# Performance work log

Measured on AMD Instinct MI355X. Metric: run time of the kernel, lower is better.

The kernel has to match this reference:

```python
import jax, jax.numpy as jnp
import numpy as np

B, N, C, H, R, E = 64, 512, 64, 8, 17, 21
HD = C // H
BETA = 0.01


def setup_inputs() -> dict:
    key = jax.random.key(0)
    ks = jax.random.split(key, 13)
    s = 0.02
    x = jax.random.normal(ks[0], (B, N, C), jnp.float32)
    ext = jax.random.normal(ks[1], (B, N, E), jnp.float32)
    # soft sector-assignment tensor (dense float, as used by the einsum)
    assignment = jax.random.uniform(ks[2], (N, N, R), jnp.float32)
    mask = jax.random.randint(ks[3], (N, R), 0, 2) == 1
    mask = mask.at[:, 0].set(False)  # guarantee >=1 unmasked sector per node
    Wq = jax.random.normal(ks[4], (C, C), jnp.float32) * s
    Wkv = jax.random.normal(ks[5], (2 * C, C), jnp.float32) * s
    relative_bias = jax.random.normal(ks[6], (H, 1, R), jnp.float32)
    W1 = jax.random.normal(ks[7], (64, E), jnp.float32) * s
    b1 = jnp.zeros((64,), jnp.float32)
    W2 = jax.random.normal(ks[8], (H * R, 64), jnp.float32) * s
    b2 = jnp.zeros((H * R,), jnp.float32)
    Wp = jax.random.normal(ks[9], (C, C), jnp.float32) * s
    bp = jnp.zeros((C,), jnp.float32)
    return dict(x=x, ext=ext, assignment=assignment, Wq=Wq, Wkv=Wkv,
                relative_bias=relative_bias, W1=W1, b1=b1, W2=W2, b2=b2,
                Wp=Wp, bp=bp, mask=mask)


def reference(x, ext, assignment, Wq, Wkv, relative_bias, W1, b1, W2, b2, Wp, bp, mask):
    scale = HD ** (-0.5)
    # sector gather: [B,N,C] x [N,N,R] -> [B,N,R,C]
    pre_kv = jnp.einsum('bnc,mnr->bmrc', x, assignment)
    # projections (torch Linear: y = x @ W^T)
    q = (x @ Wq.T).reshape(B, N, H, HD)                 # per-token single query
    kv = pre_kv @ Wkv.T                                  # [B,N,R,2C]
    k, v = jnp.split(kv, 2, axis=-1)
    k = k.reshape(B, N, R, H, HD)
    v = v.reshape(B, N, R, H, HD)
    # tiny 1xR attention per (b,n,h)
    attn = jnp.einsum('bnhd,bnrhd->bnhr', q, k) * scale
    attn = attn + relative_bias[:, 0, :][None, None]     # [H,R] broadcast
    # ext modulation
    ext_imp = jax.nn.relu(ext @ W1.T + b1) @ W2.T + b2   # [B,N,H*R] (dropout=eval)
    attn = attn + BETA * ext_imp.reshape(B, N, H, R)
    attn = jnp.where(mask[None, :, None, :], -jnp.inf, attn)
    p = jax.nn.softmax(attn, axis=-1)
    out = jnp.einsum('bnhr,bnrhd->bnhd', p, v).reshape(B, N, C)
    return out @ Wp.T + bp
```

## Files before the change

kernel.cpp:

```cpp
#include <hip/hip_runtime.h>
#include <hip/hip_bf16.h>

typedef __bf16 bf16x8 __attribute__((ext_vector_type(8)));
typedef float f32x4 __attribute__((ext_vector_type(4)));

#define NN 512
#define NR 17

#define SWZ(row, b) (((((b) >> 4) ^ ((row) & 7)) << 4) | ((b) & 15))

__device__ __forceinline__ __bf16 f2b(float f) {
  __hip_bfloat16 h = __float2bfloat16(f);
  return __builtin_bit_cast(__bf16, h);
}

__device__ __forceinline__ void gload_lds16(const void* g, void* l) {
  __builtin_amdgcn_global_load_lds(
      (const __attribute__((address_space(1))) void*)g,
      (__attribute__((address_space(3))) void*)l, 16, 0, 0);
}

__global__ __launch_bounds__(256) void pack_A(const float* __restrict__ a,
                                              __hip_bfloat16* __restrict__ A2) {
  __shared__ __hip_bfloat16 T[NR * 136];
  const int m = blockIdx.y;
  const int n0 = blockIdx.x * 128;
  const float* src = a + (size_t)m * (NN * NR) + (size_t)n0 * NR;
  for (int t = threadIdx.x; t < 128 * NR; t += 256) {
    int i = t / NR;
    int r = t - i * NR;
    T[r * 136 + i] = __float2bfloat16(src[t]);
  }
  __syncthreads();
  for (int t = threadIdx.x; t < NR * 128; t += 256) {
    int r = t >> 7;
    int i = t & 127;
    A2[((size_t)m * NR + r) * NN + n0 + i] = T[r * 136 + i];
  }
}

__global__ __launch_bounds__(256) void pack_X(const float* __restrict__ x,
                                              __hip_bfloat16* __restrict__ XT,
                                              __hip_bfloat16* __restrict__ XR) {
  __shared__ __hip_bfloat16 T[64 * 136];
  const int by = blockIdx.y;
  const int n0 = blockIdx.x * 128;
  const float* src = x + ((size_t)by * NN + n0) * 64;
  for (int t = threadIdx.x; t < 128 * 64; t += 256) {
    int i = t >> 6;
    int c = t & 63;
    __hip_bfloat16 v = __float2bfloat16(src[t]);
    T[c * 136 + i] = v;
    XR[((size_t)by * NN + n0 + i) * 64 + c] = v;
  }
  __syncthreads();
  for (int t = threadIdx.x; t < 64 * 128; t += 256) {
    int c = t >> 7;
    int i = t & 127;
    XT[((size_t)by * 64 + c) * NN + n0 + i] = T[c * 136 + i];
  }
}

__global__ __launch_bounds__(256) void prep_w(const float* __restrict__ Wq,
                                              const float* __restrict__ Wkv,
                                              const float* __restrict__ Wp,
                                              __hip_bfloat16* __restrict__ WQK,
                                              __hip_bfloat16* __restrict__ WVP) {
  const int base = blockIdx.x * 512 + threadIdx.x;
#pragma unroll
  for (int k = 0; k < 2; ++k) {
    const int idx = base + k * 256;
    {
      const int i = idx & 63, row = idx >> 6, h = row >> 6, c = row & 63;
      float a = 0.f;
#pragma unroll
      for (int d = 0; d < 8; ++d) a += Wq[(h * 8 + d) * 64 + i] * Wkv[(h * 8 + d) * 64 + c];
      WQK[idx] = __float2bfloat16(a * 0.35355339059327373f);
    }
    {
      const int hc = idx & 511, j = idx >> 9, h = hc >> 6, c = hc & 63;
      float a = 0.f;
#pragma unroll
      for (int d = 0; d < 8; ++d)
        a += Wkv[4096 + (h * 8 + d) * 64 + c] * Wp[j * 64 + (h * 8 + d)];
      WVP[idx] = __float2bfloat16(a);
    }
  }
}

#define PREKV_NWG 2176
__global__ __launch_bounds__(256) void gemm_prekv(const __hip_bfloat16* __restrict__ A2,
                                                  const __hip_bfloat16* __restrict__ XT,
                                                  __hip_bfloat16* __restrict__ pkv) {
  __shared__ char As[16384];
  __shared__ char Bs[16384];
  const int tid = threadIdx.x;
  const int wave = tid >> 6;
  const int lane = tid & 63;
  const int flat = blockIdx.y * gridDim.x + blockIdx.x;
  const int s = (flat & 7) * (PREKV_NWG / 8) + (flat >> 3);
  const int rowBase = (s >> 5) * 128;
  const int colBase = (s & 31) * 128;
  const int wrow0 = (wave >> 1) * 64;
  const int wcol0 = (wave & 1) * 64;
  const int lrow8 = lane >> 3;
  const int gslot = lane & 7;
  const int gsrc = gslot ^ lrow8;

  f32x4 acc[4][4];
#pragma unroll
  for (int i = 0; i < 4; ++i)
#pragma unroll
    for (int j = 0; j < 4; ++j) acc[i][j] = (f32x4)0.0f;

  const int fr = lane & 15;
  const int kg = lane >> 4;

  for (int kt = 0; kt < NN; kt += 64) {
#pragma unroll
    for (int cc = 0; cc < 4; ++cc) {
      const int r0 = wave * 32 + cc * 8;
      gload_lds16(A2 + ((size_t)(rowBase + r0 + lrow8) * NN + kt + gsrc * 8), As + r0 * 128);
      gload_lds16(XT + ((size_t)(colBase + r0 + lrow8) * NN + kt + gsrc * 8), Bs + r0 * 128);
    }
    __syncthreads();
#pragma unroll
    for (int kk = 0; kk < 2; ++kk) {
      bf16x8 av[4], bv[4];
#pragma unroll
      for (int mi = 0; mi < 4; ++mi) {
        const int row = wrow0 + mi * 16 + fr;
        const int slot = (kk * 4 + kg) ^ (row & 7);
        av[mi] = *(const bf16x8*)(As + row * 128 + slot * 16);
      }
#pragma unroll
      for (int ni = 0; ni < 4; ++ni) {
        const int row = wcol0 + ni * 16 + fr;
        const int slot = (kk * 4 + kg) ^ (row & 7);
        bv[ni] = *(const bf16x8*)(Bs + row * 128 + slot * 16);
      }
#pragma unroll
      for (int mi = 0; mi < 4; ++mi)
#pragma unroll
        for (int ni = 0; ni < 4; ++ni)
          acc[mi][ni] =
              __builtin_amdgcn_mfma_f32_16x16x32_bf16(av[mi], bv[ni], acc[mi][ni], 0, 0, 0);
    }
    __syncthreads();
  }

  const int rq = lane >> 4;
#pragma unroll
  for (int mi = 0; mi < 4; ++mi) {
#pragma unroll
    for (int ni = 0; ni < 4; ++ni) {
#pragma unroll
      for (int reg = 0; reg < 4; ++reg) {
        const int gi = rowBase + wrow0 + mi * 16 + rq * 4 + reg;
        const int gj = colBase + wcol0 + ni * 16 + fr;
        const unsigned m = (unsigned)gi / 17u;
        const unsigned r = (unsigned)gi - m * 17u;
        const int bb = gj >> 6;
        const int c = gj & 63;
        pkv[(((size_t)bb * NN + m) * NR + r) * 64 + c] = __float2bfloat16(acc[mi][ni][reg]);
      }
    }
  }
}

__global__ __launch_bounds__(256) void ei_kernel(const float* __restrict__ ext,
                                                 const float* __restrict__ W1p,
                                                 const float* __restrict__ b1p,
                                                 const float* __restrict__ W2p,
                                                 const float* __restrict__ b2p,
                                                 const float* __restrict__ rbp,
                                                 const int* __restrict__ maskp,
                                                 float* __restrict__ EIF) {
  __shared__ float exts[64 * 21];
  __shared__ float W1s[64 * 21];
  __shared__ __hip_bfloat16 Hl[64 * 72];
  const int tid = threadIdx.x;
  const int tblk = blockIdx.x * 64;
  for (int i = tid; i < 64 * 21; i += 256) {
    exts[i] = ext[(size_t)tblk * 21 + i];
    W1s[i] = W1p[i];
  }
  __syncthreads();
  const int wave = tid >> 6, lane = tid & 63;
#pragma unroll
  for (int k = 0; k < 16; ++k) {
    const int tl = k * 4 + wave;
    float a = b1p[lane];
#pragma unroll
    for (int e = 0; e < 21; ++e) a += exts[tl * 21 + e] * W1s[lane * 21 + e];
    Hl[tl * 72 + lane] = __float2bfloat16(fmaxf(a, 0.f));
  }
  __syncthreads();
  const int fr = lane & 15, kg = lane >> 4;
  const __bf16* Hb = (const __bf16*)Hl;
  bf16x8 a0 = *(const bf16x8*)(Hb + (wave * 16 + fr) * 72 + kg * 8);
  bf16x8 a1 = *(const bf16x8*)(Hb + (wave * 16 + fr) * 72 + 32 + kg * 8);
#pragma unroll
  for (int tile = 0; tile < 9; ++tile) {
    const int o = tile * 16 + fr;
    bf16x8 bv0 = (bf16x8)f2b(0.0f), bv1 = (bf16x8)f2b(0.0f);
    if (o < 136) {
#pragma unroll
      for (int jj = 0; jj < 8; ++jj) {
        bv0[jj] = f2b(W2p[o * 64 + kg * 8 + jj]);
        bv1[jj] = f2b(W2p[o * 64 + 32 + kg * 8 + jj]);
      }
    }
    f32x4 acc = (f32x4)0.0f;
    acc = __builtin_amdgcn_mfma_f32_16x16x32_bf16(a0, bv0, acc, 0, 0, 0);
    acc = __builtin_amdgcn_mfma_f32_16x16x32_bf16(a1, bv1, acc, 0, 0, 0);
    if (o < 136) {
      const int h = (o * 241) >> 12;
      const int r = o - h * 17;
      const float rbo = rbp[o], b2o = b2p[o];
#pragma unroll
      for (int reg = 0; reg < 4; ++reg) {
        const int tl = tblk + wave * 16 + kg * 4 + reg;
        const int m = tl & (NN - 1);
        float v = maskp[m * NR + r] ? -1e30f : (rbo + 0.01f * (acc[reg] + b2o));
        EIF[(size_t)tl * 136 + o] = v;
      }
    }
  }
}

__global__ __launch_bounds__(256, 2) void attn_mega(
    const __hip_bfloat16* __restrict__ XRp, const __hip_bfloat16* __restrict__ WQKp,
    const __hip_bfloat16* __restrict__ WVPp, const __hip_bfloat16* __restrict__ pkvB,
    const float* __restrict__ eifB, const float* __restrict__ bpp,
    float* __restrict__ outp) {
  extern __shared__ char smem[];
  char* qws = smem;
  char* Ts = smem + 32768;
  const int tid = threadIdx.x;
  const int wave = tid >> 6;
  const int lane = tid & 63;
  const int fr = lane & 15;
  const int kg = lane >> 4;
  const int t0 = blockIdx.x * 32;
  char* pT = smem + 65536 + wave * 4096;

  {
    const int rt = wave >> 1;
    const int ct0 = (wave & 1) * 16;
    bf16x8 a0 = *(const bf16x8*)((const __bf16*)XRp + (size_t)(t0 + rt * 16 + fr) * 64 + kg * 8);
    bf16x8 a1 =
        *(const bf16x8*)((const __bf16*)XRp + (size_t)(t0 + rt * 16 + fr) * 64 + 32 + kg * 8);
#pragma unroll
    for (int ci = 0; ci < 16; ++ci) {
      const int ct = ct0 + ci;
      f32x4 acc = (f32x4)0.0f;
      bf16x8 b0 = *(const bf16x8*)((const __bf16*)WQKp + (size_t)(ct * 16 + fr) * 64 + kg * 8);
      bf16x8 b1 =
          *(const bf16x8*)((const __bf16*)WQKp + (size_t)(ct * 16 + fr) * 64 + 32 + kg * 8);
      acc = __builtin_amdgcn_mfma_f32_16x16x32_bf16(a0, b0, acc, 0, 0, 0);
      acc = __builtin_amdgcn_mfma_f32_16x16x32_bf16(a1, b1, acc, 0, 0, 0);
#pragma unroll
      for (int reg = 0; reg < 4; ++reg) {
        const int row = rt * 16 + kg * 4 + reg;
        const int col = ct * 16 + fr;
        *(__hip_bfloat16*)(qws + row * 1024 + SWZ(row, col * 2)) = __float2bfloat16(acc[reg]);
      }
    }
  }

  {
    bf16x8 z = (bf16x8)f2b(0.0f);
#pragma unroll
    for (int j = 0; j < 4; ++j) *(bf16x8*)(pT + lane * 64 + j * 16) = z;
  }
  __syncthreads();

  for (int i = 0; i < 8; ++i) {
    const int tl = wave * 8 + i;
    const size_t tg = (size_t)t0 + tl;
    const __bf16* pk = (const __bf16*)pkvB + tg * 1088;

    bf16x8 v0 = *(const bf16x8*)(pk + lane * 8);
    bf16x8 v1 = *(const bf16x8*)(pk + 512 + lane * 8);
    __bf16 vt = pk[1024 + lane];
    {
      const int r0 = lane >> 3;
      const int cb = (lane & 7) * 8;
#pragma unroll
      for (int j = 0; j < 8; ++j) {
        const int c = cb + j;
        const int sl0 = (0 ^ ((c >> 2) & 3)) << 4;
        const int sl1 = (1 ^ ((c >> 2) & 3)) << 4;
        *(__bf16*)(pT + c * 64 + sl0 + r0 * 2) = v0[j];
        *(__bf16*)(pT + c * 64 + sl1 + r0 * 2) = v1[j];
      }
      const int c = lane;
      *(__bf16*)(pT + c * 64 + ((2 ^ ((c >> 2) & 3)) << 4)) = vt;
    }

    f32x4 slo = (f32x4)0.0f, shi = (f32x4)0.0f;
#pragma unroll
    for (int kk = 0; kk < 2; ++kk) {
      const int g = fr * 8 + kk * 4 + kg;
      bf16x8 av = *(const bf16x8*)(qws + tl * 1024 + ((g ^ (tl & 7)) << 4));
      bf16x8 blo = *(const bf16x8*)(pk + fr * 64 + kk * 32 + kg * 8);
      bf16x8 bhi = (bf16x8)f2b(0.0f);
      if (fr == 0) bhi = *(const bf16x8*)(pk + 1024 + kk * 32 + kg * 8);
      slo = __builtin_amdgcn_mfma_f32_16x16x32_bf16(av, blo, slo, 0, 0, 0);
      shi = __builtin_amdgcn_mfma_f32_16x16x32_bf16(av, bhi, shi, 0, 0, 0);
    }

    const float* eif = eifB + tg * 136;
    float plo[4], phi[4];
#pragma unroll
    for (int reg = 0; reg < 4; ++reg) {
      const int h = kg * 4 + reg;
      float llo = slo[reg] + eif[h * 17 + fr];
      float lhi = (fr == 0) ? (shi[reg] + eif[h * 17 + 16]) : -1e30f;
      float mx = fmaxf(llo, lhi);
      mx = fmaxf(mx, __shfl_xor(mx, 1));
      mx = fmaxf(mx, __shfl_xor(mx, 2));
      mx = fmaxf(mx, __shfl_xor(mx, 4));
      mx = fmaxf(mx, __shfl_xor(mx, 8));
      float el = __expf(llo - mx);
      float eh = __expf(lhi - mx);
      float sm = el + eh;
      sm += __shfl_xor(sm, 1);
      sm += __shfl_xor(sm, 2);
      sm += __shfl_xor(sm, 4);
      sm += __shfl_xor(sm, 8);
      const float iv = 1.0f / sm;
      plo[reg] = el * iv;
      phi[reg] = eh * iv;
    }

#pragma unroll
    for (int reg = 0; reg < 4; ++reg) {
      const int h = kg * 4 + reg;
      *(__hip_bfloat16*)(Ts + tl * 1024 + SWZ(tl, (h * 32 + fr) * 2)) =
          __float2bfloat16(plo[reg]);
      *(__hip_bfloat16*)(Ts + tl * 1024 + SWZ(tl, (h * 32 + 16 + fr) * 2)) =
          __float2bfloat16(phi[reg]);
    }
    bf16x8 ap = *(const bf16x8*)(Ts + tl * 1024 + (((fr * 4 + kg) ^ (tl & 7)) << 4));

#pragma unroll
    for (int ni = 0; ni < 4; ++ni) {
      const int c = ni * 16 + fr;
      bf16x8 bv = *(const bf16x8*)(pT + c * 64 + ((kg ^ ((c >> 2) & 3)) << 4));
      f32x4 o = __builtin_amdgcn_mfma_f32_16x16x32_bf16(ap, bv, (f32x4)0.0f, 0, 0, 0);
      if (kg < 2) {
#pragma unroll
        for (int reg = 0; reg < 4; ++reg) {
          const int h = kg * 4 + reg;
          *(__hip_bfloat16*)(Ts + tl * 1024 + SWZ(tl, (h * 64 + c) * 2)) =
              __float2bfloat16(o[reg]);
        }
      }
    }
  }
  __syncthreads();

  {
    const int rt = wave >> 1;
    const int ct_base = (wave & 1) * 2;
#pragma unroll
    for (int cj = 0; cj < 2; ++cj) {
      const int ct = ct_base + cj;
      f32x4 acc = (f32x4)0.0f;
#pragma unroll
      for (int kk = 0; kk < 16; ++kk) {
        const int row = rt * 16 + fr;
        bf16x8 a = *(const bf16x8*)(Ts + row * 1024 + (((kk * 4 + kg) ^ (row & 7)) << 4));
        bf16x8 b = *(const bf16x8*)((const __bf16*)WVPp + (size_t)(ct * 16 + fr) * 512 +
                                    kk * 32 + kg * 8);
        acc = __builtin_amdgcn_mfma_f32_16x16x32_bf16(a, b, acc, 0, 0, 0);
      }
      const float bpv = bpp[ct * 16 + fr];
#pragma unroll
      for (int reg = 0; reg < 4; ++reg)
        outp[(size_t)(t0 + rt * 16 + kg * 4 + reg) * 64 + ct * 16 + fr] = acc[reg] + bpv;
    }
  }
}

extern "C" void kernel_launch(void* const* d_in, const int* in_sizes, int n_in, void* d_out,
                              int out_size, void* d_ws, size_t ws_size, hipStream_t stream) {
  const float* x = (const float*)d_in[0];
  const float* ext = (const float*)d_in[1];
  const float* assign = (const float*)d_in[2];
  const float* Wq = (const float*)d_in[3];
  const float* Wkv = (const float*)d_in[4];
  const float* rb = (const float*)d_in[5];
  const float* W1 = (const float*)d_in[6];
  const float* b1 = (const float*)d_in[7];
  const float* W2 = (const float*)d_in[8];
  const float* b2 = (const float*)d_in[9];
  const float* Wp = (const float*)d_in[10];
  const float* bp = (const float*)d_in[11];
  const int* mask = (const int*)d_in[12];
  float* out = (float*)d_out;

  char* ws = (char*)d_ws;
  __hip_bfloat16* A2 = (__hip_bfloat16*)(ws + 0);
  __hip_bfloat16* WQK = (__hip_bfloat16*)(ws + 8912896);
  __hip_bfloat16* WVP = (__hip_bfloat16*)(ws + 8978432);
  __hip_bfloat16* XT = (__hip_bfloat16*)(ws + 9043968);
  __hip_bfloat16* XR = (__hip_bfloat16*)(ws + 13238272);
  __hip_bfloat16* PKV = (__hip_bfloat16*)(ws + 17432576);
  float* EIF = (float*)(ws + 88735744);
  if (ws_size < (size_t)106565632) return;

  hipLaunchKernelGGL(pack_A, dim3(4, 512), dim3(256), 0, stream, assign, A2);
  hipLaunchKernelGGL(prep_w, dim3(64), dim3(256), 0, stream, Wq, Wkv, Wp, WQK, WVP);
  hipLaunchKernelGGL(pack_X, dim3(4, 64), dim3(256), 0, stream, x, XT, XR);
  hipLaunchKernelGGL(gemm_prekv, dim3(32, 68), dim3(256), 0, stream, A2, XT, PKV);
  hipLaunchKernelGGL(ei_kernel, dim3(512), dim3(256), 0, stream, ext, W1, b1, W2, b2, rb, mask,
                     EIF);
  hipFuncSetAttribute((const void*)attn_mega, hipFuncAttributeMaxDynamicSharedMemorySize, 81920);
  hipLaunchKernelGGL(attn_mega, dim3(1024), dim3(256), 81920, stream, XR, WQK, WVP, PKV, EIF, bp,
                     out);
}
```

Before: 266.5 us.

## Skip masked sector rows in pre-KV GEMM and restructure attention kernel

Adds a mask-scan kernel that compacts the unmasked (node, sector) rows into an index list, and the pre-KV GEMM now computes only those rows, roughly halving its work. The attention kernel is rewritten to handle 16 tokens per block with static shared memory and 4 blocks per CU. It uses register-resident score and PV MFMAs with shuffles instead of an LDS transpose, and prefetches the next token's K/V rows. The ext-bias buffer becomes bf16 with a relayout to cut traffic. Masked rows of PKV are no longer written, so correctness relies on the -1e30 bias zeroing their probabilities and on those stale rows holding no NaN or Inf from previous workspace contents.

```diff
diff --git a/kernel.cpp b/kernel.cpp
--- a/kernel.cpp
+++ b/kernel.cpp
@@ -9,9 +9,15 @@
 
 #define SWZ(row, b) (((((b) >> 4) ^ ((row) & 7)) << 4) | ((b) & 15))
 
+__device__ __forceinline__ float bf2f(__hip_bfloat16 v) { return __bfloat162float(v); }
 __device__ __forceinline__ __bf16 f2b(float f) {
   __hip_bfloat16 h = __float2bfloat16(f);
   return __builtin_bit_cast(__bf16, h);
+}
+__device__ __forceinline__ unsigned pkbf(float a, float b) {
+  unsigned ua = (unsigned)__builtin_bit_cast(unsigned short, __float2bfloat16(a));
+  unsigned ub = (unsigned)__builtin_bit_cast(unsigned short, __float2bfloat16(b));
+  return ua | (ub << 16);
 }
 
 __device__ __forceinline__ void gload_lds16(const void* g, void* l) {
@@ -88,25 +94,63 @@
   }
 }
 
-#define PREKV_NWG 2176
+__global__ __launch_bounds__(512) void mask_scan(const int* __restrict__ maskp,
+                                                 int* __restrict__ rowsp,
+                                                 int* __restrict__ metap) {
+  __shared__ int sc[512];
+  const int tid = threadIdx.x;
+  int c = 0;
+#pragma unroll
+  for (int r = 0; r < NR; ++r) c += (maskp[tid * NR + r] == 0) ? 1 : 0;
+  sc[tid] = c;
+  __syncthreads();
+  for (int s = 1; s < 512; s <<= 1) {
+    int v = (tid >= s) ? sc[tid - s] : 0;
+    __syncthreads();
+    sc[tid] += v;
+    __syncthreads();
+  }
+  int idx = sc[tid] - c;
+#pragma unroll
+  for (int r = 0; r < NR; ++r)
+    if (maskp[tid * NR + r] == 0) rowsp[idx++] = tid * NR + r;
+  if (tid == 511) {
+    const int total = sc[511];
+    const int padded = (total + 127) & ~127;
+    for (int i = total; i < padded; ++i) rowsp[i] = 0;
+    metap[0] = padded;
+  }
+}
+
 __global__ __launch_bounds__(256) void gemm_prekv(const __hip_bfloat16* __restrict__ A2,
                                                   const __hip_bfloat16* __restrict__ XT,
+                                                  const int* __restrict__ rowsp,
+                                                  const int* __restrict__ metap,
                                                   __hip_bfloat16* __restrict__ pkv) {
   __shared__ char As[16384];
   __shared__ char Bs[16384];
+  const int padded = metap[0];
+  const int nwg = (padded >> 7) * 32;
+  const int flat = blockIdx.y * gridDim.x + blockIdx.x;
+  if (flat >= nwg) return;
+  const int s = (flat & 7) * (nwg >> 3) + (flat >> 3);
+  const int rowBase = (s >> 5) * 128;
+  const int colBase = (s & 31) * 128;
+
   const int tid = threadIdx.x;
   const int wave = tid >> 6;
   const int lane = tid & 63;
-  const int flat = blockIdx.y * gridDim.x + blockIdx.x;
-  const int s = (flat & 7) * (PREKV_NWG / 8) + (flat >> 3);
-  const int rowBase = (s >> 5) * 128;
-  const int colBase = (s & 31) * 128;
   const int wrow0 = (wave >> 1) * 64;
   const int wcol0 = (wave & 1) * 64;
   const int lrow8 = lane >> 3;
   const int gslot = lane & 7;
   const int gsrc = gslot ^ lrow8;
 
+  int arow[4];
+#pragma unroll
+  for (int cc = 0; cc < 4; ++cc)
+    arow[cc] = rowsp[rowBase + wave * 32 + cc * 8 + lrow8];
+
   f32x4 acc[4][4];
 #pragma unroll
   for (int i = 0; i < 4; ++i)
@@ -120,7 +164,7 @@
 #pragma unroll
     for (int cc = 0; cc < 4; ++cc) {
       const int r0 = wave * 32 + cc * 8;
-      gload_lds16(A2 + ((size_t)(rowBase + r0 + lrow8) * NN + kt + gsrc * 8), As + r0 * 128);
+      gload_lds16(A2 + ((size_t)arow[cc] * NN + kt + gsrc * 8), As + r0 * 128);
       gload_lds16(XT + ((size_t)(colBase + r0 + lrow8) * NN + kt + gsrc * 8), Bs + r0 * 128);
     }
     __syncthreads();
@@ -157,9 +201,10 @@
 #pragma unroll
       for (int reg = 0; reg < 4; ++reg) {
         const int gi = rowBase + wrow0 + mi * 16 + rq * 4 + reg;
+        const int grow = rowsp[gi];
+        const unsigned m = (unsigned)grow / 17u;
+        const unsigned r = (unsigned)grow - m * 17u;
         const int gj = colBase + wcol0 + ni * 16 + fr;
-        const unsigned m = (unsigned)gi / 17u;
-        const unsigned r = (unsigned)gi - m * 17u;
         const int bb = gj >> 6;
         const int c = gj & 63;
         pkv[(((size_t)bb * NN + m) * NR + r) * 64 + c] = __float2bfloat16(acc[mi][ni][reg]);
@@ -175,7 +220,7 @@
                                                  const float* __restrict__ b2p,
                                                  const float* __restrict__ rbp,
                                                  const int* __restrict__ maskp,
-                                                 float* __restrict__ EIF) {
+                                                 __hip_bfloat16* __restrict__ EIF) {
   __shared__ float exts[64 * 21];
   __shared__ float W1s[64 * 21];
   __shared__ __hip_bfloat16 Hl[64 * 72];
@@ -217,43 +262,40 @@
     if (o < 136) {
       const int h = (o * 241) >> 12;
       const int r = o - h * 17;
+      const int noff = (r < 16) ? ((r >> 2) * 64 + h * 4 + (r & 3)) : (256 + h);
       const float rbo = rbp[o], b2o = b2p[o];
 #pragma unroll
       for (int reg = 0; reg < 4; ++reg) {
         const int tl = tblk + wave * 16 + kg * 4 + reg;
         const int m = tl & (NN - 1);
         float v = maskp[m * NR + r] ? -1e30f : (rbo + 0.01f * (acc[reg] + b2o));
-        EIF[(size_t)tl * 136 + o] = v;
-      }
-    }
-  }
-}
-
-__global__ __launch_bounds__(256, 2) void attn_mega(
+        EIF[(size_t)tl * 272 + noff] = __float2bfloat16(v);
+      }
+    }
+  }
+}
+
+__global__ __launch_bounds__(256, 4) void attn_mega(
     const __hip_bfloat16* __restrict__ XRp, const __hip_bfloat16* __restrict__ WQKp,
     const __hip_bfloat16* __restrict__ WVPp, const __hip_bfloat16* __restrict__ pkvB,
-    const float* __restrict__ eifB, const float* __restrict__ bpp,
+    const __hip_bfloat16* __restrict__ eifB, const float* __restrict__ bpp,
     float* __restrict__ outp) {
-  extern __shared__ char smem[];
-  char* qws = smem;
-  char* Ts = smem + 32768;
+  __shared__ char qws[16 * 1024];
+  __shared__ char Ts[16 * 1024];
   const int tid = threadIdx.x;
   const int wave = tid >> 6;
   const int lane = tid & 63;
   const int fr = lane & 15;
   const int kg = lane >> 4;
-  const int t0 = blockIdx.x * 32;
-  char* pT = smem + 65536 + wave * 4096;
+  const int h8 = fr & 7;
+  const int t0 = blockIdx.x * 16;
 
   {
-    const int rt = wave >> 1;
-    const int ct0 = (wave & 1) * 16;
-    bf16x8 a0 = *(const bf16x8*)((const __bf16*)XRp + (size_t)(t0 + rt * 16 + fr) * 64 + kg * 8);
-    bf16x8 a1 =
-        *(const bf16x8*)((const __bf16*)XRp + (size_t)(t0 + rt * 16 + fr) * 64 + 32 + kg * 8);
-#pragma unroll
-    for (int ci = 0; ci < 16; ++ci) {
-      const int ct = ct0 + ci;
+    bf16x8 a0 = *(const bf16x8*)((const __bf16*)XRp + (size_t)(t0 + fr) * 64 + kg * 8);
+    bf16x8 a1 = *(const bf16x8*)((const __bf16*)XRp + (size_t)(t0 + fr) * 64 + 32 + kg * 8);
+#pragma unroll
+    for (int ci = 0; ci < 8; ++ci) {
+      const int ct = wave * 8 + ci;
       f32x4 acc = (f32x4)0.0f;
       bf16x8 b0 = *(const bf16x8*)((const __bf16*)WQKp + (size_t)(ct * 16 + fr) * 64 + kg * 8);
       bf16x8 b1 =
@@ -262,100 +304,101 @@
       acc = __builtin_amdgcn_mfma_f32_16x16x32_bf16(a1, b1, acc, 0, 0, 0);
 #pragma unroll
       for (int reg = 0; reg < 4; ++reg) {
-        const int row = rt * 16 + kg * 4 + reg;
+        const int row = kg * 4 + reg;
         const int col = ct * 16 + fr;
         *(__hip_bfloat16*)(qws + row * 1024 + SWZ(row, col * 2)) = __float2bfloat16(acc[reg]);
       }
     }
   }
+  __syncthreads();
 
   {
-    bf16x8 z = (bf16x8)f2b(0.0f);
-#pragma unroll
-    for (int j = 0; j < 4; ++j) *(bf16x8*)(pT + lane * 64 + j * 16) = z;
-  }
-  __syncthreads();
-
-  for (int i = 0; i < 8; ++i) {
-    const int tl = wave * 8 + i;
-    const size_t tg = (size_t)t0 + tl;
-    const __bf16* pk = (const __bf16*)pkvB + tg * 1088;
-
-    bf16x8 v0 = *(const bf16x8*)(pk + lane * 8);
-    bf16x8 v1 = *(const bf16x8*)(pk + 512 + lane * 8);
-    __bf16 vt = pk[1024 + lane];
-    {
-      const int r0 = lane >> 3;
-      const int cb = (lane & 7) * 8;
+    const __bf16* pk0 = (const __bf16*)pkvB + (size_t)(t0 + wave * 4) * 1088;
+    bf16x8 nalo0 = *(const bf16x8*)(pk0 + fr * 64 + kg * 8);
+    bf16x8 nalo1 = *(const bf16x8*)(pk0 + fr * 64 + 32 + kg * 8);
+    bf16x8 nahi0 = *(const bf16x8*)(pk0 + (16 + fr) * 64 + kg * 8);
+    bf16x8 nahi1 = *(const bf16x8*)(pk0 + (16 + fr) * 64 + 32 + kg * 8);
+
+    for (int i = 0; i < 4; ++i) {
+      const int tl = wave * 4 + i;
+      const size_t tg = (size_t)t0 + tl;
+      const __bf16* pk = (const __bf16*)pkvB + tg * 1088;
+
+      bf16x8 alo0 = nalo0, alo1 = nalo1, ahi0 = nahi0, ahi1 = nahi1;
+      if (i < 3) {
+        const __bf16* pkn = pk + 1088;
+        nalo0 = *(const bf16x8*)(pkn + fr * 64 + kg * 8);
+        nalo1 = *(const bf16x8*)(pkn + fr * 64 + 32 + kg * 8);
+        nahi0 = *(const bf16x8*)(pkn + (16 + fr) * 64 + kg * 8);
+        nahi1 = *(const bf16x8*)(pkn + (16 + fr) * 64 + 32 + kg * 8);
+      }
+
+      bf16x8 bq0 = *(const bf16x8*)(qws + tl * 1024 + (((h8 * 8 + kg) ^ (tl & 7)) << 4));
+      bf16x8 bq1 = *(const bf16x8*)(qws + tl * 1024 + (((h8 * 8 + 4 + kg) ^ (tl & 7)) << 4));
+      f32x4 slo = (f32x4)0.0f, shi = (f32x4)0.0f;
+      slo = __builtin_amdgcn_mfma_f32_16x16x32_bf16(alo0, bq0, slo, 0, 0, 0);
+      slo = __builtin_amdgcn_mfma_f32_16x16x32_bf16(alo1, bq1, slo, 0, 0, 0);
+      shi = __builtin_amdgcn_mfma_f32_16x16x32_bf16(ahi0, bq0, shi, 0, 0, 0);
+      shi = __builtin_amdgcn_mfma_f32_16x16x32_bf16(ahi1, bq1, shi, 0, 0, 0);
+
+      const __bf16* gb = pk + kg * 512 + fr;
+      bf16x8 av0, av1, av2, av3;
 #pragma unroll
       for (int j = 0; j < 8; ++j) {
-        const int c = cb + j;
-        const int sl0 = (0 ^ ((c >> 2) & 3)) << 4;
-        const int sl1 = (1 ^ ((c >> 2) & 3)) << 4;
-        *(__bf16*)(pT + c * 64 + sl0 + r0 * 2) = v0[j];
-        *(__bf16*)(pT + c * 64 + sl1 + r0 * 2) = v1[j];
-      }
-      const int c = lane;
-      *(__bf16*)(pT + c * 64 + ((2 ^ ((c >> 2) & 3)) << 4)) = vt;
-    }
-
-    f32x4 slo = (f32x4)0.0f, shi = (f32x4)0.0f;
-#pragma unroll
-    for (int kk = 0; kk < 2; ++kk) {
-      const int g = fr * 8 + kk * 4 + kg;
-      bf16x8 av = *(const bf16x8*)(qws + tl * 1024 + ((g ^ (tl & 7)) << 4));
-      bf16x8 blo = *(const bf16x8*)(pk + fr * 64 + kk * 32 + kg * 8);
-      bf16x8 bhi = (bf16x8)f2b(0.0f);
-      if (fr == 0) bhi = *(const bf16x8*)(pk + 1024 + kk * 32 + kg * 8);
-      slo = __builtin_amdgcn_mfma_f32_16x16x32_bf16(av, blo, slo, 0, 0, 0);
-      shi = __builtin_amdgcn_mfma_f32_16x16x32_bf16(av, bhi, shi, 0, 0, 0);
-    }
-
-    const float* eif = eifB + tg * 136;
-    float plo[4], phi[4];
-#pragma unroll
-    for (int reg = 0; reg < 4; ++reg) {
-      const int h = kg * 4 + reg;
-      float llo = slo[reg] + eif[h * 17 + fr];
-      float lhi = (fr == 0) ? (shi[reg] + eif[h * 17 + 16]) : -1e30f;
-      float mx = fmaxf(llo, lhi);
-      mx = fmaxf(mx, __shfl_xor(mx, 1));
-      mx = fmaxf(mx, __shfl_xor(mx, 2));
-      mx = fmaxf(mx, __shfl_xor(mx, 4));
-      mx = fmaxf(mx, __shfl_xor(mx, 8));
-      float el = __expf(llo - mx);
-      float eh = __expf(lhi - mx);
-      float sm = el + eh;
-      sm += __shfl_xor(sm, 1);
-      sm += __shfl_xor(sm, 2);
-      sm += __shfl_xor(sm, 4);
-      sm += __shfl_xor(sm, 8);
+        av0[j] = gb[j * 64];
+        av1[j] = gb[j * 64 + 16];
+        av2[j] = gb[j * 64 + 32];
+        av3[j] = gb[j * 64 + 48];
+      }
+
+      const __hip_bfloat16* eb = eifB + tg * 272;
+      ushort4 ev = *(const ushort4*)((const unsigned short*)eb + kg * 64 + h8 * 4);
+      const float ef0 = bf2f(__builtin_bit_cast(__hip_bfloat16, ev.x));
+      const float ef1 = bf2f(__builtin_bit_cast(__hip_bfloat16, ev.y));
+      const float ef2 = bf2f(__builtin_bit_cast(__hip_bfloat16, ev.z));
+      const float ef3 = bf2f(__builtin_bit_cast(__hip_bfloat16, ev.w));
+      const float e16v = bf2f(eb[256 + h8]);
+
+      const float s0 = slo[0] + ef0, s1 = slo[1] + ef1, s2 = slo[2] + ef2, s3 = slo[3] + ef3;
+      const float s16 = shi[0] + e16v;
+      float mx = fmaxf(fmaxf(s0, s1), fmaxf(s2, s3));
+      mx = fmaxf(mx, (kg == 0) ? s16 : -3.0e38f);
+      mx = fmaxf(mx, __shfl_xor(mx, 16));
+      mx = fmaxf(mx, __shfl_xor(mx, 32));
+      const float e0 = __expf(s0 - mx), e1 = __expf(s1 - mx);
+      const float e2 = __expf(s2 - mx), e3 = __expf(s3 - mx);
+      const float e16 = (kg == 0) ? __expf(s16 - mx) : 0.f;
+      float sm = e0 + e1 + e2 + e3 + e16;
+      sm += __shfl_xor(sm, 16);
+      sm += __shfl_xor(sm, 32);
       const float iv = 1.0f / sm;
-      plo[reg] = el * iv;
-      phi[reg] = eh * iv;
-    }
-
-#pragma unroll
-    for (int reg = 0; reg < 4; ++reg) {
-      const int h = kg * 4 + reg;
-      *(__hip_bfloat16*)(Ts + tl * 1024 + SWZ(tl, (h * 32 + fr) * 2)) =
-          __float2bfloat16(plo[reg]);
-      *(__hip_bfloat16*)(Ts + tl * 1024 + SWZ(tl, (h * 32 + 16 + fr) * 2)) =
-          __float2bfloat16(phi[reg]);
-    }
-    bf16x8 ap = *(const bf16x8*)(Ts + tl * 1024 + (((fr * 4 + kg) ^ (tl & 7)) << 4));
-
-#pragma unroll
-    for (int ni = 0; ni < 4; ++ni) {
-      const int c = ni * 16 + fr;
-      bf16x8 bv = *(const bf16x8*)(pT + c * 64 + ((kg ^ ((c >> 2) & 3)) << 4));
-      f32x4 o = __builtin_amdgcn_mfma_f32_16x16x32_bf16(ap, bv, (f32x4)0.0f, 0, 0, 0);
-      if (kg < 2) {
-#pragma unroll
-        for (int reg = 0; reg < 4; ++reg) {
-          const int h = kg * 4 + reg;
-          *(__hip_bfloat16*)(Ts + tl * 1024 + SWZ(tl, (h * 64 + c) * 2)) =
-              __float2bfloat16(o[reg]);
+
+      const unsigned pk01 = pkbf(e0 * iv, e1 * iv);
+      const unsigned pk23 = pkbf(e2 * iv, e3 * iv);
+      const unsigned pk16 = pkbf(e16 * iv, 0.f);
+      const int src0 = (fr + 32 * kg) & 63;
+      const int src1 = (fr + 16 + 32 * kg) & 63;
+      unsigned w0 = (unsigned)__shfl((int)pk01, src0);
+      unsigned w1 = (unsigned)__shfl((int)pk23, src0);
+      unsigned w2 = (unsigned)__shfl((int)pk01, src1);
+      unsigned w3 = (unsigned)__shfl((int)pk23, src1);
+      const unsigned w16 = (unsigned)__shfl((int)pk16, fr);
+      if (kg == 2) { w0 = w16; w1 = 0; w2 = 0; w3 = 0; }
+      if (kg == 3) { w0 = 0; w1 = 0; w2 = 0; w3 = 0; }
+      uint4 apu;
+      apu.x = w0; apu.y = w1; apu.z = w2; apu.w = w3;
+      const bf16x8 ap = __builtin_bit_cast(bf16x8, apu);
+
+#pragma unroll
+      for (int ni = 0; ni < 4; ++ni) {
+        const bf16x8 av = (ni == 0) ? av0 : (ni == 1) ? av1 : (ni == 2) ? av2 : av3;
+        f32x4 o = __builtin_amdgcn_mfma_f32_16x16x32_bf16(av, ap, (f32x4)0.0f, 0, 0, 0);
+        if (fr < 8) {
+          uint2 val;
+          val.x = pkbf(o[0], o[1]);
+          val.y = pkbf(o[2], o[3]);
+          const int byte = fr * 128 + ni * 32 + kg * 8;
+          *(uint2*)(Ts + tl * 1024 + SWZ(tl, byte)) = val;
         }
       }
     }
@@ -363,25 +406,19 @@
   __syncthreads();
 
   {
-    const int rt = wave >> 1;
-    const int ct_base = (wave & 1) * 2;
-#pragma unroll
-    for (int cj = 0; cj < 2; ++cj) {
-      const int ct = ct_base + cj;
-      f32x4 acc = (f32x4)0.0f;
-#pragma unroll
-      for (int kk = 0; kk < 16; ++kk) {
-        const int row = rt * 16 + fr;
-        bf16x8 a = *(const bf16x8*)(Ts + row * 1024 + (((kk * 4 + kg) ^ (row & 7)) << 4));
-        bf16x8 b = *(const bf16x8*)((const __bf16*)WVPp + (size_t)(ct * 16 + fr) * 512 +
-                                    kk * 32 + kg * 8);
-        acc = __builtin_amdgcn_mfma_f32_16x16x32_bf16(a, b, acc, 0, 0, 0);
-      }
-      const float bpv = bpp[ct * 16 + fr];
-#pragma unroll
-      for (int reg = 0; reg < 4; ++reg)
-        outp[(size_t)(t0 + rt * 16 + kg * 4 + reg) * 64 + ct * 16 + fr] = acc[reg] + bpv;
-    }
+    const int ct = wave;
+    f32x4 acc = (f32x4)0.0f;
+#pragma unroll
+    for (int kk = 0; kk < 16; ++kk) {
+      bf16x8 a = *(const bf16x8*)(Ts + fr * 1024 + (((kk * 4 + kg) ^ (fr & 7)) << 4));
+      bf16x8 b = *(const bf16x8*)((const __bf16*)WVPp + (size_t)(ct * 16 + fr) * 512 +
+                                  kk * 32 + kg * 8);
+      acc = __builtin_amdgcn_mfma_f32_16x16x32_bf16(a, b, acc, 0, 0, 0);
+    }
+    const float bpv = bpp[ct * 16 + fr];
+#pragma unroll
+    for (int reg = 0; reg < 4; ++reg)
+      outp[(size_t)(t0 + kg * 4 + reg) * 64 + ct * 16 + fr] = acc[reg] + bpv;
   }
 }
 
@@ -409,16 +446,19 @@
   __hip_bfloat16* XT = (__hip_bfloat16*)(ws + 9043968);
   __hip_bfloat16* XR = (__hip_bfloat16*)(ws + 13238272);
   __hip_bfloat16* PKV = (__hip_bfloat16*)(ws + 17432576);
-  float* EIF = (float*)(ws + 88735744);
-  if (ws_size < (size_t)106565632) return;
+  int* rowsBuf = (int*)(ws + 88743936);
+  int* metaBuf = (int*)(ws + 88778752);
+  __hip_bfloat16* EIF = (__hip_bfloat16*)(ws + 88779008);
+  if (ws_size < (size_t)106604800) return;
 
   hipLaunchKernelGGL(pack_A, dim3(4, 512), dim3(256), 0, stream, assign, A2);
   hipLaunchKernelGGL(prep_w, dim3(64), dim3(256), 0, stream, Wq, Wkv, Wp, WQK, WVP);
   hipLaunchKernelGGL(pack_X, dim3(4, 64), dim3(256), 0, stream, x, XT, XR);
-  hipLaunchKernelGGL(gemm_prekv, dim3(32, 68), dim3(256), 0, stream, A2, XT, PKV);
+  hipLaunchKernelGGL(mask_scan, dim3(1), dim3(512), 0, stream, mask, rowsBuf, metaBuf);
+  hipLaunchKernelGGL(gemm_prekv, dim3(32, 68), dim3(256), 0, stream, A2, XT, rowsBuf, metaBuf,
+                     PKV);
   hipLaunchKernelGGL(ei_kernel, dim3(512), dim3(256), 0, stream, ext, W1, b1, W2, b2, rb, mask,
                      EIF);
-  hipFuncSetAttribute((const void*)attn_mega, hipFuncAttributeMaxDynamicSharedMemorySize, 81920);
-  hipLaunchKernelGGL(attn_mega, dim3(1024), dim3(256), 81920, stream, XR, WQK, WVP, PKV, EIF, bp,
+  hipLaunchKernelGGL(attn_mega, dim3(2048), dim3(256), 0, stream, XR, WQK, WVP, PKV, EIF, bp,
                      out);
 }
```

New measurement: 228.6 us. -14.2%, faster.
